# Kernel optimization log

Measured on AMD Instinct MI355X. Metric: run time of the kernel, lower is better.

Reference implementation:

```python
import jax, jax.numpy as jnp
import numpy as np

DIM, HEADS, HEAD_DIM, P = 256, 8, 64, 16
N = P * P          # 256 tokens
H2 = HEADS // 2    # heads in SDPA branch
SCALE = HEAD_DIM ** -0.5
BN_EPS = 1e-5


def _depthwise(x, w, kh, kw):
    # x: (b, DIM, P, P), w: (DIM, kh*kw) depthwise kernel -> same spatial size
    rhs = w.reshape(DIM, 1, kh, kw)
    return jax.lax.conv_general_dilated(
        x, rhs, window_strides=(1, 1),
        padding=((kh // 2, kh // 2), (kw // 2, kw // 2)),
        dimension_numbers=('NCHW', 'OIHW', 'NCHW'),
        feature_group_count=DIM)


def setup_inputs() -> dict:
    key = jax.random.key(0)
    ks = jax.random.split(key, 8)
    b = 128
    return {
        'x': jax.random.normal(ks[0], (b, N, DIM), jnp.float32),
        'bn_gamma': jax.random.uniform(ks[1], (DIM,), jnp.float32, 0.5, 1.5),
        'bn_beta': jax.random.normal(ks[2], (DIM,), jnp.float32) * 0.1,
        'bn_mean': jax.random.normal(ks[3], (DIM,), jnp.float32) * 0.1,
        'bn_var': jax.random.uniform(ks[4], (DIM,), jnp.float32, 0.5, 1.5),
        'w_qkv': jax.random.normal(ks[5], (DIM, 6), jnp.float32) * 0.1,
        'w_qs': jax.random.normal(ks[6], (DIM, 3), jnp.float32) * 0.1,
        'w_ks': jax.random.normal(ks[7], (DIM, 3), jnp.float32) * 0.1,
    }


def reference(x, bn_gamma, bn_beta, bn_mean, bn_var, w_qkv, w_qs, w_ks):
    b = x.shape[0]
    # raw contiguous view (b,n,d) -> (b,dim,p,p), as in the torch code
    xi = x.reshape(b, DIM, P, P)
    inv = jax.lax.rsqrt(bn_var + BN_EPS)
    xb = jax.nn.relu(((xi - bn_mean[None, :, None, None]) * (bn_gamma * inv)[None, :, None, None])
                     + bn_beta[None, :, None, None])
    # grouped 1x1 conv (groups=DIM, 6 out-channels per group)
    qkv = (xb[:, :, None, :, :] * w_qkv[None, :, :, None, None]).reshape(b, DIM * 6, P, P)
    # raw view (b, 6*dim, p, p) -> (b, n, 6*dim)
    qkv = qkv.reshape(b, N, 6 * DIM)
    q, k, v = jnp.split(qkv, 3, axis=-1)  # each (b, n, 2*dim)

    def to_heads(t):
        return t.reshape(b, N, HEADS, HEAD_DIM).transpose(0, 2, 1, 3)  # b h n d

    q, k, v = to_heads(q), to_heads(k), to_heads(v)
    q1, k1, v1 = q[:, :H2], k[:, :H2], v[:, :H2]
    # raw reshape (b, H2, n, head_dim) -> (b, dim, p, p)
    q2 = q[:, H2:].reshape(b, DIM, P, P)
    k2 = k[:, H2:].reshape(b, DIM, P, P)
    v2 = v[:, H2:].reshape(b, DIM, P, P)
    q2 = _depthwise(q2, w_qs, 1, 3)
    k2 = _depthwise(k2, w_ks, 3, 1)
    res2 = (q2 + k2 + v2).reshape(b, N, DIM)

    scores = jnp.einsum('bhid,bhjd->bhij', q1, k1) * SCALE
    attn = jax.nn.softmax(scores, axis=-1)
    out = jnp.einsum('bhij,bhjd->bhid', attn, v1)
    out = out.transpose(0, 2, 1, 3).reshape(b, N, H2 * HEAD_DIM)  # (b, n, dim)

    res = jnp.concatenate([out, res2], axis=2)  # (b, n, 2*dim)
    # AdaptiveAvgPool1d(dim) on length 2*dim == pairwise mean
    return res.reshape(b, N, DIM, 2).mean(axis=-1)
```

## Files before the change

kernel.cpp:

```cpp
#include <hip/hip_runtime.h>

typedef __bf16 bf16;
typedef __attribute__((ext_vector_type(8))) __bf16 bf16x8;
typedef __attribute__((ext_vector_type(4))) __bf16 bf16x4;
typedef __attribute__((ext_vector_type(4))) float floatx4;

#define MFMA16(a,b,c) __builtin_amdgcn_mfma_f32_16x16x32_bf16((a),(b),(c),0,0,0)

__device__ __forceinline__ float fast_exp2(float xv) {
#if __has_builtin(__builtin_amdgcn_exp2f)
  return __builtin_amdgcn_exp2f(xv);
#else
  return exp2f(xv);
#endif
}

__device__ __forceinline__ void ld8f(const bf16* p, float* dst) {
  bf16x8 v = *(const bf16x8*)p;
#pragma unroll
  for (int i = 0; i < 8; ++i) dst[i] = (float)v[i];
}

__global__ __launch_bounds__(512, 4) void fused_kernel(
    const float* __restrict__ x,
    const float* __restrict__ bn_gamma, const float* __restrict__ bn_beta,
    const float* __restrict__ bn_mean, const float* __restrict__ bn_var,
    const float* __restrict__ w_qkv, const float* __restrict__ w_qs,
    const float* __restrict__ w_ks,
    float* __restrict__ out)
{
  __shared__ __align__(16) char smem[72704];
  bf16 (*Abf)[72]  = (bf16(*)[72])smem;
  bf16 (*VtF)[264] = (bf16(*)[264])(smem + 36864);
  float* ckA = (float*)(smem + 70656);
  float* cvA = (float*)(smem + 71680);
  float* scT = (float*)(smem + 36864);
  float* bsT = (float*)(smem + 36864 + 1024);

  const int t  = threadIdx.x;
  const int bb = blockIdx.x >> 2;
  const int h  = blockIdx.x & 3;

  if (t < 256) {
    float inv = rsqrtf(bn_var[t] + 1e-5f);
    float sc  = bn_gamma[t] * inv;
    scT[t] = sc;
    bsT[t] = bn_beta[t] - bn_mean[t] * sc;
    ckA[t] = w_qkv[t*6+2];
    cvA[t] = w_qkv[t*6+4];
  }
  __syncthreads();

  const float* xb = x + (size_t)bb * 65536 + h * 64;
  {
    const int rsub = t >> 4, ch = t & 15;
#pragma unroll
    for (int i2 = 0; i2 < 8; ++i2) {
      int n = i2*32 + rsub;
      float4 v = *(const float4*)(xb + (size_t)n*256 + ch*4);
      float sc = scT[n], bs = bsT[n];
      bf16x4 bv;
      bv.x = (bf16)fmaxf(fmaf(v.x, sc, bs), 0.f);
      bv.y = (bf16)fmaxf(fmaf(v.y, sc, bs), 0.f);
      bv.z = (bf16)fmaxf(fmaf(v.z, sc, bs), 0.f);
      bv.w = (bf16)fmaxf(fmaf(v.w, sc, bs), 0.f);
      *(bf16x4*)&Abf[n][ch*4] = bv;
    }
  }
  __syncthreads();

  {
    const int j32 = t & 31, g = t >> 5;
#pragma unroll
    for (int jt = 0; jt < 8; ++jt) {
      int j = jt*32 + j32;
      bf16x4 v = *(const bf16x4*)&Abf[j][g*4];
      float cv = cvA[j];
      VtF[g*4+0][j] = (bf16)((float)v.x * cv);
      VtF[g*4+1][j] = (bf16)((float)v.y * cv);
      VtF[g*4+2][j] = (bf16)((float)v.z * cv);
      VtF[g*4+3][j] = (bf16)((float)v.w * cv);
    }
  }
  __syncthreads();

  const int lane = t & 63;
  const int wid  = t >> 6;
  const int q    = lane >> 4;
  const int c    = lane & 15;
  const int R    = wid * 32;
  const int jp   = ((c >> 2) << 3) + (c & 3);

  float cqv[2];
  cqv[0] = w_qkv[(R + c)*6]      * 0.18033688f;
  cqv[1] = w_qkv[(R + 16 + c)*6] * 0.18033688f;

  bf16x8 bi0[2], bi1[2];
#pragma unroll
  for (int it = 0; it < 2; ++it) {
    const bf16* bp = &Abf[R + 16*it + c][0];
    bi0[it] = *(const bf16x8*)(bp + 8*q);
    bi1[it] = *(const bf16x8*)(bp + 32 + 8*q);
  }

  floatx4 oacc[2][4];
  float lacc[2] = {0.f, 0.f};
#pragma unroll
  for (int it = 0; it < 2; ++it)
#pragma unroll
    for (int et = 0; et < 4; ++et)
      oacc[it][et] = (floatx4){0.f,0.f,0.f,0.f};

  for (int jt = 0; jt < 8; ++jt) {
    const int j0 = jt * 32;
    const int jr = j0 + jp;

    bf16x8 aj00 = *(const bf16x8*)&Abf[jr][8*q];
    bf16x8 aj01 = *(const bf16x8*)&Abf[jr][32 + 8*q];
    bf16x8 aj10 = *(const bf16x8*)&Abf[jr + 4][8*q];
    bf16x8 aj11 = *(const bf16x8*)&Abf[jr + 4][32 + 8*q];
    floatx4 ckv0 = *(const floatx4*)&ckA[j0 + 8*q];
    floatx4 ckv1 = *(const floatx4*)&ckA[j0 + 8*q + 4];

    bf16x8 pa[2];
#pragma unroll
    for (int it = 0; it < 2; ++it) {
      floatx4 s0 = (floatx4){0.f,0.f,0.f,0.f};
      floatx4 s1 = (floatx4){0.f,0.f,0.f,0.f};
      s0 = MFMA16(aj00, bi0[it], s0); s0 = MFMA16(aj01, bi1[it], s0);
      s1 = MFMA16(aj10, bi0[it], s1); s1 = MFMA16(aj11, bi1[it], s1);
      bf16x8 pv;
      float ps = 0.f;
#pragma unroll
      for (int r = 0; r < 4; ++r) {
        float e0v = fast_exp2(fminf(cqv[it]*ckv0[r]*s0[r], 80.f));
        float e1v = fast_exp2(fminf(cqv[it]*ckv1[r]*s1[r], 80.f));
        ps += e0v + e1v;
        pv[r]     = (bf16)e0v;
        pv[4 + r] = (bf16)e1v;
      }
      lacc[it] += ps;
      pa[it] = pv;
    }

#pragma unroll
    for (int et = 0; et < 4; ++et) {
      bf16x8 vb = *(const bf16x8*)&VtF[16*et + c][j0 + 8*q];
      oacc[0][et] = MFMA16(pa[0], vb, oacc[0][et]);
      oacc[1][et] = MFMA16(pa[1], vb, oacc[1][et]);
    }
  }

#pragma unroll
  for (int it = 0; it < 2; ++it) {
    float v = lacc[it];
    v += __shfl_xor(v, 16, 64);
    v += __shfl_xor(v, 32, 64);
    lacc[it] = v;
  }

  float* outA = out + ((size_t)bb*256)*256 + h*32;
#pragma unroll
  for (int it = 0; it < 2; ++it) {
#pragma unroll
    for (int r = 0; r < 4; ++r) {
      float lsrc = __shfl(lacc[it], 4*q + r, 64);
      float linv = 0.5f / lsrc;
      int n = R + 16*it + 4*q + r;
#pragma unroll
      for (int et = 0; et < 4; ++et) {
        float v = oacc[it][et][r];
        float v2 = v + __shfl_xor(v, 1, 64);
        if (!(lane & 1))
          outA[(size_t)n*256 + 8*et + (c>>1)] = v2 * linv;
      }
    }
  }

  {
    const int ci = t >> 3, sub = t & 7, qq = sub >> 1, uh = sub & 1;
    const int C  = h*64 + ci;
    const int a  = 4*ci + qq;
    const int e0 = 32*uh;

    float qs0 = w_qs[C*3+0], qs1 = w_qs[C*3+1], qs2 = w_qs[C*3+2];
    float ks0 = w_ks[C*3+0], ks1 = w_ks[C*3+1], ks2 = w_ks[C*3+2];
    float wq1a = w_qkv[a*6+1], wk1a = w_qkv[a*6+3], wv1a = w_qkv[a*6+5];
    float wcf = fmaf(ks1, wk1a, wv1a);

    float wmx = 0.f;
    if (uh) wmx = ks0 * wk1a;
    else if (qq > 0) wmx = ks0 * w_qkv[(a-1)*6+3];
    float wmh = ks0 * wk1a;
    float wpl = ks2 * wk1a;
    float wpx = 0.f;
    if (!uh) wpx = ks2 * wk1a;
    else if (qq < 3) wpx = ks2 * w_qkv[(a+1)*6+3];

    float Xc[32], Xl[16], Xr[16];
#pragma unroll
    for (int m = 0; m < 4; ++m) ld8f(&Abf[a][e0 + 8*m], &Xc[8*m]);
    if (uh) {
      ld8f(&Abf[a][16], &Xl[0]); ld8f(&Abf[a][24], &Xl[8]);
    } else if (qq > 0) {
      ld8f(&Abf[a-1][48], &Xl[0]); ld8f(&Abf[a-1][56], &Xl[8]);
    } else {
#pragma unroll
      for (int i = 0; i < 16; ++i) Xl[i] = 0.f;
    }
    if (!uh) {
      ld8f(&Abf[a][32], &Xr[0]); ld8f(&Abf[a][40], &Xr[8]);
    } else if (qq < 3) {
      ld8f(&Abf[a+1][0], &Xr[0]); ld8f(&Abf[a+1][8], &Xr[8]);
    } else {
#pragma unroll
      for (int i = 0; i < 16; ++i) Xr[i] = 0.f;
    }

    float res[16];
    float prev = 0.f;
#pragma unroll
    for (int k = 0; k < 32; ++k) {
      float fc = Xc[k];
      float qv = qs1 * fc;
      if (k & 15)         qv = fmaf(qs0, Xc[k-1], qv);
      if ((k & 15) != 15) qv = fmaf(qs2, Xc[k+1], qv);
      float acc = fmaf(wq1a, qv, wcf * fc);
      float tm = (k < 16) ? Xl[k]     : Xc[k-16];
      float wm = (k < 16) ? wmx       : wmh;
      acc = fmaf(wm, tm, acc);
      float tp = (k < 16) ? Xc[k+16]  : Xr[k-16];
      float wp = (k < 16) ? wpl       : wpx;
      acc = fmaf(wp, tp, acc);
      if (k & 1) res[k>>1] = 0.5f * (prev + acc);
      else       prev = acc;
    }

    float* outC = out + ((size_t)(bb*256 + C))*256 + 128 + 32*qq + 16*uh;
#pragma unroll
    for (int m = 0; m < 4; ++m) {
      float4 o4;
      o4.x = res[4*m]; o4.y = res[4*m+1]; o4.z = res[4*m+2]; o4.w = res[4*m+3];
      *(float4*)(outC + 4*m) = o4;
    }
  }
}

extern "C" void kernel_launch(void* const* d_in, const int* in_sizes, int n_in,
                              void* d_out, int out_size, void* d_ws, size_t ws_size,
                              hipStream_t stream) {
  (void)in_sizes; (void)n_in; (void)out_size; (void)d_ws; (void)ws_size;
  const float* x    = (const float*)d_in[0];
  const float* g    = (const float*)d_in[1];
  const float* be   = (const float*)d_in[2];
  const float* mn   = (const float*)d_in[3];
  const float* vr   = (const float*)d_in[4];
  const float* wqkv = (const float*)d_in[5];
  const float* wqs  = (const float*)d_in[6];
  const float* wks  = (const float*)d_in[7];
  float* out = (float*)d_out;

  fused_kernel<<<dim3(512), dim3(512), 0, stream>>>(x, g, be, mn, vr, wqkv, wqs, wks, out);
}
```

Baseline: 107.1 us.

## Fold q scale into operands, compute softmax denominators via MFMA, stagger key tiles

```diff
diff --git a/kernel.cpp b/kernel.cpp
--- a/kernel.cpp
+++ b/kernel.cpp
@@ -3,6 +3,7 @@
 typedef __bf16 bf16;
 typedef __attribute__((ext_vector_type(8))) __bf16 bf16x8;
 typedef __attribute__((ext_vector_type(4))) __bf16 bf16x4;
+typedef __attribute__((ext_vector_type(2))) __bf16 bf16x2;
 typedef __attribute__((ext_vector_type(4))) float floatx4;
 
 #define MFMA16(a,b,c) __builtin_amdgcn_mfma_f32_16x16x32_bf16((a),(b),(c),0,0,0)
@@ -70,16 +71,20 @@
   __syncthreads();
 
   {
-    const int j32 = t & 31, g = t >> 5;
-#pragma unroll
-    for (int jt = 0; jt < 8; ++jt) {
-      int j = jt*32 + j32;
-      bf16x4 v = *(const bf16x4*)&Abf[j][g*4];
-      float cv = cvA[j];
-      VtF[g*4+0][j] = (bf16)((float)v.x * cv);
-      VtF[g*4+1][j] = (bf16)((float)v.y * cv);
-      VtF[g*4+2][j] = (bf16)((float)v.z * cv);
-      VtF[g*4+3][j] = (bf16)((float)v.w * cv);
+    const int J  = t & 127;
+    const int eg = t >> 7;
+    const bf16* r0 = &Abf[2*J][16*eg];
+    const bf16* r1 = &Abf[2*J + 1][16*eg];
+    bf16x8 a0l = *(const bf16x8*)r0, a0h = *(const bf16x8*)(r0 + 8);
+    bf16x8 a1l = *(const bf16x8*)r1, a1h = *(const bf16x8*)(r1 + 8);
+    float cv0 = cvA[2*J], cv1 = cvA[2*J + 1];
+#pragma unroll
+    for (int e = 0; e < 8; ++e) {
+      union { bf16x2 hh; unsigned u; } wl, wh;
+      wl.hh = (bf16x2){(bf16)((float)a0l[e]*cv0), (bf16)((float)a1l[e]*cv1)};
+      wh.hh = (bf16x2){(bf16)((float)a0h[e]*cv0), (bf16)((float)a1h[e]*cv1)};
+      *(unsigned*)&VtF[16*eg + e][2*J]     = wl.u;
+      *(unsigned*)&VtF[16*eg + 8 + e][2*J] = wh.u;
     }
   }
   __syncthreads();
@@ -91,36 +96,53 @@
   const int R    = wid * 32;
   const int jp   = ((c >> 2) << 3) + (c & 3);
 
-  float cqv[2];
-  cqv[0] = w_qkv[(R + c)*6]      * 0.18033688f;
-  cqv[1] = w_qkv[(R + 16 + c)*6] * 0.18033688f;
-
+  float cqs[2];
+  cqs[0] = w_qkv[(R + c)*6]      * 0.18033688f;
+  cqs[1] = w_qkv[(R + 16 + c)*6] * 0.18033688f;
   bf16x8 bi0[2], bi1[2];
 #pragma unroll
   for (int it = 0; it < 2; ++it) {
     const bf16* bp = &Abf[R + 16*it + c][0];
-    bi0[it] = *(const bf16x8*)(bp + 8*q);
-    bi1[it] = *(const bf16x8*)(bp + 32 + 8*q);
-  }
+    bf16x8 r0 = *(const bf16x8*)(bp + 8*q);
+    bf16x8 r1 = *(const bf16x8*)(bp + 32 + 8*q);
+#pragma unroll
+    for (int e = 0; e < 8; ++e) {
+      bi0[it][e] = (bf16)((float)r0[e] * cqs[it]);
+      bi1[it][e] = (bf16)((float)r1[e] * cqs[it]);
+    }
+  }
+
+  bf16x8 vbONE;
+#pragma unroll
+  for (int e = 0; e < 8; ++e) vbONE[e] = (bf16)1.0f;
 
   floatx4 oacc[2][4];
-  float lacc[2] = {0.f, 0.f};
-#pragma unroll
-  for (int it = 0; it < 2; ++it)
+  floatx4 oaccL[2];
+#pragma unroll
+  for (int it = 0; it < 2; ++it) {
+    oaccL[it] = (floatx4){0.f,0.f,0.f,0.f};
 #pragma unroll
     for (int et = 0; et < 4; ++et)
       oacc[it][et] = (floatx4){0.f,0.f,0.f,0.f};
-
+  }
+
+  const int jbase = wid & 7;
+#pragma unroll 2
   for (int jt = 0; jt < 8; ++jt) {
-    const int j0 = jt * 32;
+    const int j0 = (((jt + jbase) & 7) << 5);
+
+    bf16x8 vb0 = *(const bf16x8*)&VtF[     c][j0 + 8*q];
+    bf16x8 vb1 = *(const bf16x8*)&VtF[16 + c][j0 + 8*q];
+    bf16x8 vb2 = *(const bf16x8*)&VtF[32 + c][j0 + 8*q];
+    bf16x8 vb3 = *(const bf16x8*)&VtF[48 + c][j0 + 8*q];
+
     const int jr = j0 + jp;
-
     bf16x8 aj00 = *(const bf16x8*)&Abf[jr][8*q];
     bf16x8 aj01 = *(const bf16x8*)&Abf[jr][32 + 8*q];
     bf16x8 aj10 = *(const bf16x8*)&Abf[jr + 4][8*q];
     bf16x8 aj11 = *(const bf16x8*)&Abf[jr + 4][32 + 8*q];
-    floatx4 ckv0 = *(const floatx4*)&ckA[j0 + 8*q];
-    floatx4 ckv1 = *(const floatx4*)&ckA[j0 + 8*q + 4];
+    floatx4 ck0 = *(const floatx4*)&ckA[j0 + 8*q];
+    floatx4 ck1 = *(const floatx4*)&ckA[j0 + 8*q + 4];
 
     bf16x8 pa[2];
 #pragma unroll
@@ -130,42 +152,33 @@
       s0 = MFMA16(aj00, bi0[it], s0); s0 = MFMA16(aj01, bi1[it], s0);
       s1 = MFMA16(aj10, bi0[it], s1); s1 = MFMA16(aj11, bi1[it], s1);
       bf16x8 pv;
-      float ps = 0.f;
 #pragma unroll
       for (int r = 0; r < 4; ++r) {
-        float e0v = fast_exp2(fminf(cqv[it]*ckv0[r]*s0[r], 80.f));
-        float e1v = fast_exp2(fminf(cqv[it]*ckv1[r]*s1[r], 80.f));
-        ps += e0v + e1v;
-        pv[r]     = (bf16)e0v;
-        pv[4 + r] = (bf16)e1v;
+        pv[r]     = (bf16)fast_exp2(ck0[r] * s0[r]);
+        pv[4 + r] = (bf16)fast_exp2(ck1[r] * s1[r]);
       }
-      lacc[it] += ps;
       pa[it] = pv;
     }
 
-#pragma unroll
-    for (int et = 0; et < 4; ++et) {
-      bf16x8 vb = *(const bf16x8*)&VtF[16*et + c][j0 + 8*q];
-      oacc[0][et] = MFMA16(pa[0], vb, oacc[0][et]);
-      oacc[1][et] = MFMA16(pa[1], vb, oacc[1][et]);
-    }
-  }
-
+    oaccL[0] = MFMA16(pa[0], vbONE, oaccL[0]);
+    oaccL[1] = MFMA16(pa[1], vbONE, oaccL[1]);
+
+    oacc[0][0] = MFMA16(pa[0], vb0, oacc[0][0]);
+    oacc[1][0] = MFMA16(pa[1], vb0, oacc[1][0]);
+    oacc[0][1] = MFMA16(pa[0], vb1, oacc[0][1]);
+    oacc[1][1] = MFMA16(pa[1], vb1, oacc[1][1]);
+    oacc[0][2] = MFMA16(pa[0], vb2, oacc[0][2]);
+    oacc[1][2] = MFMA16(pa[1], vb2, oacc[1][2]);
+    oacc[0][3] = MFMA16(pa[0], vb3, oacc[0][3]);
+    oacc[1][3] = MFMA16(pa[1], vb3, oacc[1][3]);
+  }
+
+  float* outA = out + ((size_t)bb*256)*256 + h*32;
 #pragma unroll
   for (int it = 0; it < 2; ++it) {
-    float v = lacc[it];
-    v += __shfl_xor(v, 16, 64);
-    v += __shfl_xor(v, 32, 64);
-    lacc[it] = v;
-  }
-
-  float* outA = out + ((size_t)bb*256)*256 + h*32;
-#pragma unroll
-  for (int it = 0; it < 2; ++it) {
 #pragma unroll
     for (int r = 0; r < 4; ++r) {
-      float lsrc = __shfl(lacc[it], 4*q + r, 64);
-      float linv = 0.5f / lsrc;
+      float linv = 0.5f / oaccL[it][r];
       int n = R + 16*it + 4*q + r;
 #pragma unroll
       for (int et = 0; et < 4; ++et) {
```

Result: faster. 105.0 us (-2.0%).
